# Optimization experiments

Measured on AMD Instinct MI355X. Metric: run time of the kernel, lower is better.

The kernel has to match this reference:

```python
import jax, jax.numpy as jnp
import numpy as np

N = 100000   # nodes per graph (protein == ligand node count, forced by cat dim=1)
E = 3200000  # edges per graph (avg degree 32)
F = 128      # input feature dim
A = 10       # action dim


def _fanin_uniform(key, shape, fanin=None):
    fanin = fanin or shape[0]
    v = 1.0 / np.sqrt(fanin)
    return jax.random.uniform(key, shape, jnp.float32, -v, v)


def setup_inputs() -> dict:
    key = jax.random.key(0)
    ks = jax.random.split(key, 24)
    inp = {
        "protein_x": jax.random.normal(ks[0], (N, F), jnp.float32),
        "protein_edges": jax.random.randint(ks[1], (2, E), 0, N, jnp.int32),
        "ligand_x": jax.random.normal(ks[2], (N, F), jnp.float32),
        "ligand_edges": jax.random.randint(ks[3], (2, E), 0, N, jnp.int32),
        "action": jax.random.normal(ks[4], (N, A), jnp.float32),
        # protein GraphConv layers
        "wp1s": _fanin_uniform(ks[5], (F, 16)),
        "wp1n": _fanin_uniform(ks[6], (F, 16)),
        "bp1": jnp.zeros((16,), jnp.float32),
        "wp2s": _fanin_uniform(ks[7], (16, 50)),
        "wp2n": _fanin_uniform(ks[8], (16, 50)),
        "bp2": jnp.zeros((50,), jnp.float32),
        # ligand GraphConv layers
        "wl1s": _fanin_uniform(ks[9], (F, 16)),
        "wl1n": _fanin_uniform(ks[10], (F, 16)),
        "bl1": jnp.zeros((16,), jnp.float32),
        "wl2s": _fanin_uniform(ks[11], (16, 50)),
        "wl2n": _fanin_uniform(ks[12], (16, 50)),
        "bl2": jnp.zeros((50,), jnp.float32),
        # MLP head
        "w_in": _fanin_uniform(ks[13], (100, 60)),
        "b_in": jnp.zeros((60,), jnp.float32),
        "w_hid": _fanin_uniform(ks[14], (60 + A, 10)),
        "b_hid": jnp.zeros((10,), jnp.float32),
        "w_out": jax.random.uniform(ks[15], (10, 1), jnp.float32, -0.003, 0.003),
        "b_out": jnp.zeros((1,), jnp.float32),
    }
    return inp


def graph_conv(x, edge_index, w_self, w_nbr, b):
    # PyG GraphConv: x_i' = x_i @ W_self + (sum_{j->i} x_j) @ W_nbr + b
    src, dst = edge_index[0], edge_index[1]
    agg = jax.ops.segment_sum(x[src], dst, num_segments=x.shape[0])  # [N, Fin]
    return x @ w_self + agg @ w_nbr + b


def reference(protein_x, protein_edges, ligand_x, ligand_edges, action,
              wp1s, wp1n, bp1, wp2s, wp2n, bp2,
              wl1s, wl1n, bl1, wl2s, wl2n, bl2,
              w_in, b_in, w_hid, b_hid, w_out, b_out):
    # protein branch (dropout is identity in eval mode)
    p = jax.nn.relu(graph_conv(protein_x, protein_edges, wp1s, wp1n, bp1))
    p = graph_conv(p, protein_edges, wp2s, wp2n, bp2)            # [N, 50]
    # ligand branch
    l = jax.nn.relu(graph_conv(ligand_x, ligand_edges, wl1s, wl1n, bl1))
    l = graph_conv(l, ligand_edges, wl2s, wl2n, bl2)             # [N, 50]
    molecule = jnp.concatenate([p, l], axis=1)                   # [N, 100]
    finger_print = jax.nn.relu(molecule @ w_in + b_in)           # [N, 60]
    policy = jnp.concatenate([finger_print, action], axis=1) @ w_hid + b_hid
    policy = jax.nn.relu(policy) @ w_out + b_out                 # [N, 1]
    return policy
```

## Files before the change

kernel.cpp:

```cpp
#include <hip/hip_runtime.h>
#include <hip/hip_bf16.h>
#include <stdint.h>


#define F_IN 128
#define NBMAX 512
#define BIN_CH 16
#define BIN_EDGES (256 * BIN_CH)
#define FINE_CAP 12288

#define OW1P  0
#define OB1P  4096
#define OW1L  4112
#define OB1L  8208
#define OC1P  8224
#define OC2P  9184
#define OC1L  10144
#define OC2L  11104
#define OBIN  12064
#define OWHID 12124
#define OBHID 12824
#define OWOUT 12834
#define OBOUT 12844
#define WBUF_FLOATS 16384

__device__ __forceinline__ float bf2f(unsigned short u) {
    union { unsigned int i; float f; } v; v.i = ((unsigned int)u) << 16; return v.f;
}
__device__ __forceinline__ float bflo(unsigned int u) {
    union { unsigned int i; float f; } v; v.i = u << 16; return v.f;
}
__device__ __forceinline__ float bfhi(unsigned int u) {
    union { unsigned int i; float f; } v; v.i = u & 0xffff0000u; return v.f;
}
__device__ __forceinline__ unsigned short f2bf(float f) {
    union { float f; unsigned int i; } v; v.f = f;
    unsigned int u = v.i;
    unsigned int r = (u + 0x7fffu + ((u >> 16) & 1u)) >> 16;
    return (unsigned short)r;
}
__device__ __forceinline__ unsigned pack2bf(float a, float b) {
    return (unsigned)f2bf(a) | ((unsigned)f2bf(b) << 16);
}
__device__ __forceinline__ float ldf(const void* p, int isf32, size_t i) {
    return isf32 ? ((const float*)p)[i] : bf2f(((const unsigned short*)p)[i]);
}

__global__ __launch_bounds__(256) void k_detect(
    const unsigned short* __restrict__ x, int nProbe, int* __restrict__ flag,
    int* __restrict__ zp, int zn)
{
    if (blockIdx.x == 0) {
        __shared__ int cnt;
        if (threadIdx.x == 0) cnt = 0;
        __syncthreads();
        int bad = 0;
        for (int i = threadIdx.x; i < nProbe; i += 256) {
            unsigned e = (x[i] >> 7) & 0xFFu;
            if (e >= 140u) bad++;
        }
        atomicAdd(&cnt, bad);
        __syncthreads();
        if (threadIdx.x == 0) *flag = (cnt > nProbe / 16) ? 1 : 0;
    } else {
        int i = (blockIdx.x - 1) * 256 + threadIdx.x;
        if (i < zn) zp[i] = 0;
    }
}


struct PW {
    const void *wp1s, *wp1n, *bp1, *wl1s, *wl1n, *bl1;
    const void *wp2s, *wp2n, *bp2, *wl2s, *wl2n, *bl2;
    const void *w_in, *b_in, *w_hid, *b_hid, *w_out, *b_out;
};

__global__ __launch_bounds__(256) void k_prepw(PW P, float* __restrict__ wb,
                                               const int* __restrict__ flag)
{
    const int isf32 = *flag;
    int t = blockIdx.x * 256 + threadIdx.x;
    int stride = gridDim.x * 256;
    for (int i = t; i < 4096; i += stride) {
        int k = i >> 5, j = i & 31;
        wb[OW1P + i] = (j < 16) ? ldf(P.wp1s, isf32, k * 16 + j)
                                : ldf(P.wp1n, isf32, k * 16 + (j - 16));
        wb[OW1L + i] = (j < 16) ? ldf(P.wl1s, isf32, k * 16 + j)
                                : ldf(P.wl1n, isf32, k * 16 + (j - 16));
    }
    for (int i = t; i < 16; i += stride) {
        wb[OB1P + i] = ldf(P.bp1, isf32, i);
        wb[OB1L + i] = ldf(P.bl1, isf32, i);
    }
    for (int i = t; i < 960; i += stride) {
        int k = i / 60, j = i % 60;
        float s1 = 0.f, s2 = 0.f;
        for (int r = 0; r < 50; ++r) {
            float wi = ldf(P.w_in, isf32, r * 60 + j);
            s1 += ldf(P.wp2s, isf32, k * 50 + r) * wi;
            s2 += ldf(P.wp2n, isf32, k * 50 + r) * wi;
        }
        wb[OC1P + i] = s1; wb[OC2P + i] = s2;
    }
    for (int i = t; i < 960; i += stride) {
        int k = i / 60, j = i % 60;
        float s1 = 0.f, s2 = 0.f;
        for (int r = 0; r < 50; ++r) {
            float wi = ldf(P.w_in, isf32, (50 + r) * 60 + j);
            s1 += ldf(P.wl2s, isf32, k * 50 + r) * wi;
            s2 += ldf(P.wl2n, isf32, k * 50 + r) * wi;
        }
        wb[OC1L + i] = s1; wb[OC2L + i] = s2;
    }
    for (int i = t; i < 60; i += stride) {
        float s = ldf(P.b_in, isf32, i);
        for (int r = 0; r < 50; ++r) {
            s += ldf(P.bp2, isf32, r) * ldf(P.w_in, isf32, r * 60 + i);
            s += ldf(P.bl2, isf32, r) * ldf(P.w_in, isf32, (50 + r) * 60 + i);
        }
        wb[OBIN + i] = s;
    }
    for (int i = t; i < 700; i += stride) wb[OWHID + i] = ldf(P.w_hid, isf32, i);
    for (int i = t; i < 10; i += stride) {
        wb[OBHID + i] = ldf(P.b_hid, isf32, i);
        wb[OWOUT + i] = ldf(P.w_out, isf32, i);
    }
    if (t == 0) wb[OBOUT] = ldf(P.b_out, isf32, 0);
}


__global__ __launch_bounds__(256) void k_bucket_hist(
    const int* __restrict__ ed0, const int* __restrict__ ed1,
    int* __restrict__ cnt, int nE)
{
    const int* ed = blockIdx.y ? ed1 : ed0;
    int* c = cnt + blockIdx.y * NBMAX;
    __shared__ int h[NBMAX];
    for (int i = threadIdx.x; i < NBMAX; i += 256) h[i] = 0;
    __syncthreads();
    int stride = gridDim.x * 256;
    for (int e = blockIdx.x * 256 + threadIdx.x; e < nE; e += stride)
        atomicAdd(&h[ed[e] >> 8], 1);
    __syncthreads();
    for (int i = threadIdx.x; i < NBMAX; i += 256)
        if (h[i]) atomicAdd(&c[i], h[i]);
}

__global__ __launch_bounds__(512) void k_bucket_scan(
    const int* __restrict__ cnt, int* __restrict__ base,
    int* __restrict__ cursor, int nb)
{
    const int* c = cnt + blockIdx.x * NBMAX;
    int* ba = base + blockIdx.x * 528;
    int* cu = cursor + blockIdx.x * NBMAX;
    __shared__ int sh[512];
    int t = threadIdx.x;
    int v = (t < nb) ? c[t] : 0;
    sh[t] = v;
    __syncthreads();
    for (int off = 1; off < 512; off <<= 1) {
        int x = (t >= off) ? sh[t - off] : 0;
        __syncthreads();
        sh[t] += x;
        __syncthreads();
    }
    int excl = sh[t] - v;
    if (t < nb) { ba[t] = excl; cu[t] = excl; }
    if (t == nb - 1) ba[nb] = excl + v;
}

__global__ __launch_bounds__(256) void k_bucket_bin(
    const int* __restrict__ es0, const int* __restrict__ ed0,
    const int* __restrict__ es1, const int* __restrict__ ed1,
    int* __restrict__ cursor, unsigned* __restrict__ pairs, int nE)
{
    const int* es = blockIdx.y ? es1 : es0;
    const int* ed = blockIdx.y ? ed1 : ed0;
    int* cur = cursor + blockIdx.y * NBMAX;
    unsigned* pr = pairs + (size_t)blockIdx.y * nE;

    __shared__ int h[NBMAX];
    __shared__ int lcur[NBMAX];
    __shared__ int sh[256];
    __shared__ unsigned stage[BIN_EDGES];
    __shared__ unsigned short stageB[BIN_EDGES];

    for (int i = threadIdx.x; i < NBMAX; i += 256) h[i] = 0;
    __syncthreads();
    int e0 = blockIdx.x * BIN_EDGES;
    int s[BIN_CH], d[BIN_CH];
#pragma unroll
    for (int k = 0; k < BIN_CH; ++k) {
        int e = e0 + k * 256 + threadIdx.x;
        if (e < nE) {
            s[k] = es[e]; d[k] = ed[e];
            atomicAdd(&h[d[k] >> 8], 1);
        } else d[k] = -1;
    }
    __syncthreads();
    {
        int t = threadIdx.x;
        int a = h[2 * t], b2 = h[2 * t + 1];
        sh[t] = a + b2;
        __syncthreads();
        for (int off = 1; off < 256; off <<= 1) {
            int x = (t >= off) ? sh[t - off] : 0;
            __syncthreads();
            sh[t] += x;
            __syncthreads();
        }
        int excl = sh[t] - (a + b2);
        lcur[2 * t] = excl;
        lcur[2 * t + 1] = excl + a;
    }
    __syncthreads();
    for (int b = threadIdx.x; b < NBMAX; b += 256) {
        int c = h[b];
        if (c) {
            int g = atomicAdd(&cur[b], c);
            h[b] = g - lcur[b];
        }
    }
    __syncthreads();
#pragma unroll
    for (int k = 0; k < BIN_CH; ++k) {
        if (d[k] >= 0) {
            int b = d[k] >> 8;
            int pos = atomicAdd(&lcur[b], 1);
            stage[pos] = ((unsigned)(d[k] & 255) << 24) | (unsigned)s[k];
            stageB[pos] = (unsigned short)b;
        }
    }
    __syncthreads();
    int total = nE - e0; if (total > BIN_EDGES) total = BIN_EDGES;
    for (int i = threadIdx.x; i < total; i += 256)
        pr[h[stageB[i]] + i] = stage[i];
}

__global__ __launch_bounds__(256) void k_bucket_fine(
    const unsigned* __restrict__ pairs, const int* __restrict__ base,
    int* __restrict__ row0, int* __restrict__ srcs0,
    int* __restrict__ row1, int* __restrict__ srcs1,
    int n, int nE, int nb)
{
    const unsigned* pr = pairs + (size_t)blockIdx.y * nE;
    const int* ba = base + blockIdx.y * 528;
    int* row = blockIdx.y ? row1 : row0;
    int* srcs = blockIdx.y ? srcs1 : srcs0;
    __shared__ int cnt[256], cur[256];
    __shared__ int stage[FINE_CAP];
    int b = blockIdx.x;
    int t = threadIdx.x;
    int s0 = ba[b], s1 = ba[b + 1];
    int m = s1 - s0;
    cnt[t] = 0;
    __syncthreads();
    for (int i = s0 + t; i < s1; i += 256)
        atomicAdd(&cnt[pr[i] >> 24], 1);
    __syncthreads();
    int c = cnt[t];
    cur[t] = c;
    __syncthreads();
    for (int off = 1; off < 256; off <<= 1) {
        int x = (t >= off) ? cur[t - off] : 0;
        __syncthreads();
        cur[t] += x;
        __syncthreads();
    }
    int excl = cur[t] - c;
    __syncthreads();
    int node = (b << 8) + t;
    if (node < n) row[node] = s0 + excl;
    if (b == nb - 1 && t == 0) row[n] = nE;
    if (m <= FINE_CAP) {
        cur[t] = excl;
        __syncthreads();
        for (int i = s0 + t; i < s1; i += 256) {
            unsigned p = pr[i];
            int slot = atomicAdd(&cur[p >> 24], 1);
            stage[slot] = (int)(p & 0xFFFFFFu);
        }
        __syncthreads();
        for (int i = t; i < m; i += 256)
            srcs[s0 + i] = stage[i];
    } else {
        cur[t] = s0 + excl;
        __syncthreads();
        for (int i = s0 + t; i < s1; i += 256) {
            unsigned p = pr[i];
            int slot = atomicAdd(&cur[p >> 24], 1);
            srcs[slot] = (int)(p & 0xFFFFFFu);
        }
    }
}


struct TArgs2 {
    const void* __restrict__ x;
    const float* __restrict__ w;
    const float* __restrict__ b;
    float* __restrict__ acc;
    void* __restrict__ nbr;
};

__global__ __launch_bounds__(512) void k_transform1(
    TArgs2 a0, TArgs2 a1, int n, const int* __restrict__ flag)
{
    TArgs2 A = blockIdx.y ? a1 : a0;
    const int isf32 = *flag;
    __shared__ unsigned char xs_raw[32768];
    const int t = threadIdx.x;
    const int tile0 = blockIdx.x * 64;

    if (isf32) {
        const float4* xg = (const float4*)A.x;
        float4* xl = (float4*)xs_raw;
#pragma unroll
        for (int i = 0; i < 4; ++i) {
            int flat = i * 512 + t;
            int row = flat >> 5, ck = flat & 31;
            if (tile0 + row < n)
                xl[row * 32 + (ck ^ (row & 7))] =
                    xg[((size_t)(tile0 + row)) * 32 + ck];
        }
    } else {
        const uint4* xg = (const uint4*)A.x;
        uint4* xl = (uint4*)xs_raw;
#pragma unroll
        for (int i = 0; i < 2; ++i) {
            int flat = i * 512 + t;
            int row = flat >> 4, ck = flat & 15;
            if (tile0 + row < n)
                xl[row * 16 + (ck ^ (row & 7))] =
                    xg[((size_t)(tile0 + row)) * 16 + ck];
        }
    }
    __syncthreads();

    const int jq = __builtin_amdgcn_readfirstlane(t >> 6);
    const int r = t & 63;
    const int node = tile0 + r;
    if (node >= n) return;
    const float* __restrict__ Wb = A.w + 4 * jq;
    const int sw = r & 7;

    float acc[4];
    if (jq < 4) {
#pragma unroll
        for (int j = 0; j < 4; ++j) acc[j] = A.b[4 * jq + j];
    } else {
#pragma unroll
        for (int j = 0; j < 4; ++j) acc[j] = 0.f;
    }

    if (isf32) {
        const float4* xl = (const float4*)xs_raw + r * 32;
        for (int kk = 0; kk < 32; ++kk) {
            float4 q = xl[kk ^ sw];
            float xv[4] = {q.x, q.y, q.z, q.w};
#pragma unroll
            for (int h = 0; h < 4; ++h) {
                const float* __restrict__ w0 = Wb + (kk * 4 + h) * 32;
#pragma unroll
                for (int j = 0; j < 4; ++j) acc[j] += xv[h] * w0[j];
            }
        }
    } else {
        const uint4* xl = (const uint4*)xs_raw + r * 16;
        for (int kk = 0; kk < 16; ++kk) {
            uint4 q = xl[kk ^ sw];
            float xv[8] = {bflo(q.x), bfhi(q.x), bflo(q.y), bfhi(q.y),
                           bflo(q.z), bfhi(q.z), bflo(q.w), bfhi(q.w)};
#pragma unroll
            for (int h = 0; h < 8; ++h) {
                const float* __restrict__ w0 = Wb + (kk * 8 + h) * 32;
#pragma unroll
                for (int j = 0; j < 4; ++j) acc[j] += xv[h] * w0[j];
            }
        }
    }

    if (jq < 4) {
        float4* a4 = (float4*)(A.acc + (size_t)node * 16);
        a4[jq] = make_float4(acc[0], acc[1], acc[2], acc[3]);
    } else {
        unsigned short* nrow = (unsigned short*)A.nbr + ((size_t)node << 4)
                               + ((jq - 4) << 2);
        *(uint2*)nrow = make_uint2(pack2bf(acc[0], acc[1]),
                                   pack2bf(acc[2], acc[3]));
    }
}

struct GArgs { const int *row, *srcs; const void* val; float* out; void* rout; };

__global__ __launch_bounds__(256) void k_gather16(
    GArgs g0, GArgs g1, int n, int selfmode, int yoff)
{
    GArgs G = (blockIdx.y + yoff) ? g1 : g0;
    int t = blockIdx.x * 256 + threadIdx.x;
    int node = t >> 2;
    if (node >= n) return;
    int c = (t & 3) << 2;
    const unsigned short* vb = (const unsigned short*)G.val;
    int rs = G.row[node], re = G.row[node + 1];
    float4 sum = make_float4(0.f, 0.f, 0.f, 0.f);
    if (selfmode) sum = *(const float4*)(G.out + ((size_t)node << 4) + c);
    int j = rs;
    for (; j + 16 <= re; j += 16) {
        int s[16];
        uint2 v[16];
#pragma unroll
        for (int u = 0; u < 16; ++u) s[u] = G.srcs[j + u];
#pragma unroll
        for (int u = 0; u < 16; ++u)
            v[u] = *(const uint2*)(vb + (((size_t)s[u]) << 4) + c);
#pragma unroll
        for (int u = 0; u < 16; ++u) {
            sum.x += bflo(v[u].x); sum.y += bfhi(v[u].x);
            sum.z += bflo(v[u].y); sum.w += bfhi(v[u].y);
        }
    }
    for (; j + 8 <= re; j += 8) {
        int s[8];
        uint2 v[8];
#pragma unroll
        for (int u = 0; u < 8; ++u) s[u] = G.srcs[j + u];
#pragma unroll
        for (int u = 0; u < 8; ++u)
            v[u] = *(const uint2*)(vb + (((size_t)s[u]) << 4) + c);
#pragma unroll
        for (int u = 0; u < 8; ++u) {
            sum.x += bflo(v[u].x); sum.y += bfhi(v[u].x);
            sum.z += bflo(v[u].y); sum.w += bfhi(v[u].y);
        }
    }
    for (; j < re; ++j) {
        uint2 v = *(const uint2*)(vb + (((size_t)G.srcs[j]) << 4) + c);
        sum.x += bflo(v.x); sum.y += bfhi(v.x);
        sum.z += bflo(v.y); sum.w += bfhi(v.y);
    }
    *(float4*)(G.out + ((size_t)node << 4) + c) = sum;
    if (selfmode) {
        unsigned short* orow = (unsigned short*)G.rout + ((size_t)node << 4) + c;
        *(uint2*)orow = make_uint2(pack2bf(fmaxf(sum.x, 0.f), fmaxf(sum.y, 0.f)),
                                   pack2bf(fmaxf(sum.z, 0.f), fmaxf(sum.w, 0.f)));
    }
}

__device__ __forceinline__ void fp_acc30(float* fp, const float* __restrict__ wb,
                                         int off, int jo,
                                         const float* __restrict__ row, bool dorelu)
{
    const float4* r4 = (const float4*)row;
    for (int kk = 0; kk < 4; ++kk) {
        float4 v = r4[kk];
        float xs[4] = {v.x, v.y, v.z, v.w};
        if (dorelu) {
            xs[0] = fmaxf(xs[0], 0.f); xs[1] = fmaxf(xs[1], 0.f);
            xs[2] = fmaxf(xs[2], 0.f); xs[3] = fmaxf(xs[3], 0.f);
        }
        const float* __restrict__ wq = wb + off + kk * 240 + jo;
#pragma unroll
        for (int h = 0; h < 4; ++h) {
#pragma unroll
            for (int j = 0; j < 30; ++j) fp[j] += xs[h] * wq[h * 60 + j];
        }
    }
}

__global__ __launch_bounds__(256) void k_headf(
    const float* __restrict__ hP, const float* __restrict__ gP,
    const float* __restrict__ hL, const float* __restrict__ gL,
    const void* __restrict__ action, const float* __restrict__ wb,
    void* __restrict__ out, int n, const int* __restrict__ flag)
{
    const int isf32 = *flag;
    __shared__ float hbuf[128][10];
    int w = threadIdx.x >> 6;
    int jh = __builtin_amdgcn_readfirstlane(w & 1);
    int slot = ((w >> 1) << 6) + (threadIdx.x & 63);
    int node = blockIdx.x * 128 + slot;
    int nodec = node < n ? node : (n - 1);
    const int jo = 30 * jh;

    float fp[30];
#pragma unroll
    for (int j = 0; j < 30; ++j) fp[j] = wb[OBIN + jo + j];

    fp_acc30(fp, wb, OC1P, jo, hP + (size_t)nodec * 16, true);
    fp_acc30(fp, wb, OC2P, jo, gP + (size_t)nodec * 16, false);
    fp_acc30(fp, wb, OC1L, jo, hL + (size_t)nodec * 16, true);
    fp_acc30(fp, wb, OC2L, jo, gL + (size_t)nodec * 16, false);

    float h[10];
#pragma unroll
    for (int j = 0; j < 10; ++j) h[j] = (jh == 0) ? wb[OBHID + j] : 0.f;
#pragma unroll
    for (int k = 0; k < 30; ++k) {
        float v = fmaxf(fp[k], 0.f);
#pragma unroll
        for (int j = 0; j < 10; ++j) h[j] += v * wb[OWHID + (jo + k) * 10 + j];
    }
    if (jh) {
#pragma unroll
        for (int j = 0; j < 10; ++j) hbuf[slot][j] = h[j];
    }
    __syncthreads();
    if (jh == 0) {
#pragma unroll
        for (int j = 0; j < 10; ++j) h[j] += hbuf[slot][j];
#pragma unroll
        for (int k = 0; k < 10; ++k) {
            float v = ldf(action, isf32, (size_t)nodec * 10 + k);
#pragma unroll
            for (int j = 0; j < 10; ++j) h[j] += v * wb[OWHID + (60 + k) * 10 + j];
        }
        float o = wb[OBOUT];
#pragma unroll
        for (int j = 0; j < 10; ++j) o += fmaxf(h[j], 0.f) * wb[OWOUT + j];
        if (node < n) {
            if (isf32) ((float*)out)[node] = o;
            else       ((unsigned short*)out)[node] = f2bf(o);
        }
    }
}

extern "C" void kernel_launch(void* const* d_in, const int* in_sizes, int n_in,
                              void* d_out, int out_size, void* d_ws, size_t ws_size,
                              hipStream_t stream)
{
    const void* px   = d_in[0];
    const int*  pe   = (const int*)d_in[1];
    const void* lx   = d_in[2];
    const int*  le   = (const int*)d_in[3];
    const void* act  = d_in[4];

    const int N = in_sizes[0] / F_IN;
    const int E = in_sizes[1] / 2;
    const int NB = (N + 255) >> 8;

    int* flag    = (int*)d_ws;
    int* cnt     = flag + 64;
    int* base    = cnt + 2 * NBMAX;
    int* cursorB = base + 2 * 528;
    float* wbuf  = (float*)(flag + 3200);
    int* rowP    = flag + 3200 + WBUF_FLOATS;
    int* srcsP   = rowP + (N + 64);
    int* rowL    = srcsP + E;
    int* srcsL   = rowL + (N + 64);
    float* dense = (float*)(srcsL + E);
    unsigned* pairs = (unsigned*)dense;

    float* accP = dense;
    float* accL = accP + (size_t)N * 16;
    float* aggP = accL + (size_t)N * 16;
    float* aggL = aggP + (size_t)N * 16;
    void*  n1P  = (void*)(aggL + (size_t)N * 16);
    void*  n1L  = (void*)((float*)n1P + (size_t)N * 8);
    void*  n2P  = (void*)((float*)n1L + (size_t)N * 8);
    void*  n2L  = (void*)((float*)n2P + (size_t)N * 8);

    const int nb64 = (N + 63) / 64;
    const int nb128 = (N + 127) / 128;
    const int gb = (N * 4 + 255) / 256;
    const int bb = (E + BIN_EDGES - 1) / BIN_EDGES;

    k_detect<<<5, 256, 0, stream>>>((const unsigned short*)px, 4096, flag,
                                    cnt, 2 * NBMAX);

    PW P{d_in[5], d_in[6], d_in[7], d_in[11], d_in[12], d_in[13],
         d_in[8], d_in[9], d_in[10], d_in[14], d_in[15], d_in[16],
         d_in[17], d_in[18], d_in[19], d_in[20], d_in[21], d_in[22]};
    k_prepw<<<32, 256, 0, stream>>>(P, wbuf, flag);

    k_bucket_hist<<<dim3(512, 2), 256, 0, stream>>>(pe + E, le + E, cnt, E);
    k_bucket_scan<<<2, 512, 0, stream>>>(cnt, base, cursorB, NB);
    k_bucket_bin<<<dim3(bb, 2), 256, 0, stream>>>(pe, pe + E, le, le + E,
                                                  cursorB, pairs, E);
    k_bucket_fine<<<dim3(NB, 2), 256, 0, stream>>>(pairs, base, rowP, srcsP,
                                                   rowL, srcsL, N, E, NB);

    TArgs2 tP{px, wbuf + OW1P, wbuf + OB1P, accP, n1P};
    TArgs2 tL{lx, wbuf + OW1L, wbuf + OB1L, accL, n1L};
    k_transform1<<<dim3(nb64, 2), 512, 0, stream>>>(tP, tL, N, flag);

    GArgs g1P{rowP, srcsP, n1P, accP, n2P}, g1L{rowL, srcsL, n1L, accL, n2L};
    k_gather16<<<dim3(gb, 2), 256, 0, stream>>>(g1P, g1L, N, 1, 0);

    GArgs g2P{rowP, srcsP, n2P, aggP, nullptr}, g2L{rowL, srcsL, n2L, aggL, nullptr};
    k_gather16<<<dim3(gb, 2), 256, 0, stream>>>(g2P, g2L, N, 0, 0);

    k_headf<<<nb128, 256, 0, stream>>>(accP, aggP, accL, aggL, act, wbuf,
                                       d_out, N, flag);
}
```

Baseline: 485.7 us.

## Merge dtype detection into weight prep, widen gather loads, unpack bf16 at staging

Removes the separate detect kernel by having every k_prepw block recompute the dtype probe and zero the counters, which saves one launch. The two gather passes now use 2 threads per node with 16-byte loads instead of 4 threads with 8-byte loads, so fewer instructions are issued per gathered neighbour row. In the transform kernel, bf16 inputs are converted to fp32 once while staging into LDS, so a single fp32 inner loop serves both dtypes. The cost is less thread parallelism in the gather and redundant probe work in every prepw block.

```diff
diff --git a/kernel.cpp b/kernel.cpp
--- a/kernel.cpp
+++ b/kernel.cpp
@@ -46,28 +46,6 @@
     return isf32 ? ((const float*)p)[i] : bf2f(((const unsigned short*)p)[i]);
 }
 
-__global__ __launch_bounds__(256) void k_detect(
-    const unsigned short* __restrict__ x, int nProbe, int* __restrict__ flag,
-    int* __restrict__ zp, int zn)
-{
-    if (blockIdx.x == 0) {
-        __shared__ int cnt;
-        if (threadIdx.x == 0) cnt = 0;
-        __syncthreads();
-        int bad = 0;
-        for (int i = threadIdx.x; i < nProbe; i += 256) {
-            unsigned e = (x[i] >> 7) & 0xFFu;
-            if (e >= 140u) bad++;
-        }
-        atomicAdd(&cnt, bad);
-        __syncthreads();
-        if (threadIdx.x == 0) *flag = (cnt > nProbe / 16) ? 1 : 0;
-    } else {
-        int i = (blockIdx.x - 1) * 256 + threadIdx.x;
-        if (i < zn) zp[i] = 0;
-    }
-}
-
 
 struct PW {
     const void *wp1s, *wp1n, *bp1, *wl1s, *wl1n, *bl1;
@@ -75,12 +53,27 @@
     const void *w_in, *b_in, *w_hid, *b_hid, *w_out, *b_out;
 };
 
-__global__ __launch_bounds__(256) void k_prepw(PW P, float* __restrict__ wb,
-                                               const int* __restrict__ flag)
-{
-    const int isf32 = *flag;
+__global__ __launch_bounds__(256) void k_prepw(
+    PW P, const unsigned short* __restrict__ px, float* __restrict__ wb,
+    int* __restrict__ flag, int* __restrict__ zp, int zn)
+{
+    __shared__ int cnt_s;
+    if (threadIdx.x == 0) cnt_s = 0;
+    __syncthreads();
+    int bad = 0;
+    for (int i = threadIdx.x; i < 4096; i += 256) {
+        unsigned e = (px[i] >> 7) & 0xFFu;
+        if (e >= 140u) bad++;
+    }
+    atomicAdd(&cnt_s, bad);
+    __syncthreads();
+    const int isf32 = (cnt_s > 4096 / 16) ? 1 : 0;
+    if (threadIdx.x == 0 && blockIdx.x == 0) *flag = isf32;
+
     int t = blockIdx.x * 256 + threadIdx.x;
     int stride = gridDim.x * 256;
+    for (int i = t; i < zn; i += stride) zp[i] = 0;
+
     for (int i = t; i < 4096; i += stride) {
         int k = i >> 5, j = i & 31;
         wb[OW1P + i] = (j < 16) ? ldf(P.wp1s, isf32, k * 16 + j)
@@ -308,13 +301,13 @@
 {
     TArgs2 A = blockIdx.y ? a1 : a0;
     const int isf32 = *flag;
-    __shared__ unsigned char xs_raw[32768];
+    __shared__ float xs[64 * 128];
     const int t = threadIdx.x;
     const int tile0 = blockIdx.x * 64;
 
     if (isf32) {
         const float4* xg = (const float4*)A.x;
-        float4* xl = (float4*)xs_raw;
+        float4* xl = (float4*)xs;
 #pragma unroll
         for (int i = 0; i < 4; ++i) {
             int flat = i * 512 + t;
@@ -325,14 +318,18 @@
         }
     } else {
         const uint4* xg = (const uint4*)A.x;
-        uint4* xl = (uint4*)xs_raw;
+        float4* xl = (float4*)xs;
 #pragma unroll
         for (int i = 0; i < 2; ++i) {
             int flat = i * 512 + t;
             int row = flat >> 4, ck = flat & 15;
-            if (tile0 + row < n)
-                xl[row * 16 + (ck ^ (row & 7))] =
-                    xg[((size_t)(tile0 + row)) * 16 + ck];
+            if (tile0 + row < n) {
+                uint4 q = xg[((size_t)(tile0 + row)) * 16 + ck];
+                float4 lo = make_float4(bflo(q.x), bfhi(q.x), bflo(q.y), bfhi(q.y));
+                float4 hi = make_float4(bflo(q.z), bfhi(q.z), bflo(q.w), bfhi(q.w));
+                xl[row * 32 + ((2 * ck) ^ (row & 7))] = lo;
+                xl[row * 32 + ((2 * ck + 1) ^ (row & 7))] = hi;
+            }
         }
     }
     __syncthreads();
@@ -353,30 +350,15 @@
         for (int j = 0; j < 4; ++j) acc[j] = 0.f;
     }
 
-    if (isf32) {
-        const float4* xl = (const float4*)xs_raw + r * 32;
-        for (int kk = 0; kk < 32; ++kk) {
-            float4 q = xl[kk ^ sw];
-            float xv[4] = {q.x, q.y, q.z, q.w};
-#pragma unroll
-            for (int h = 0; h < 4; ++h) {
-                const float* __restrict__ w0 = Wb + (kk * 4 + h) * 32;
-#pragma unroll
-                for (int j = 0; j < 4; ++j) acc[j] += xv[h] * w0[j];
-            }
-        }
-    } else {
-        const uint4* xl = (const uint4*)xs_raw + r * 16;
-        for (int kk = 0; kk < 16; ++kk) {
-            uint4 q = xl[kk ^ sw];
-            float xv[8] = {bflo(q.x), bfhi(q.x), bflo(q.y), bfhi(q.y),
-                           bflo(q.z), bfhi(q.z), bflo(q.w), bfhi(q.w)};
-#pragma unroll
-            for (int h = 0; h < 8; ++h) {
-                const float* __restrict__ w0 = Wb + (kk * 8 + h) * 32;
-#pragma unroll
-                for (int j = 0; j < 4; ++j) acc[j] += xv[h] * w0[j];
-            }
+    const float4* xl = (const float4*)xs + r * 32;
+    for (int kk = 0; kk < 32; ++kk) {
+        float4 q = xl[kk ^ sw];
+        float xv[4] = {q.x, q.y, q.z, q.w};
+#pragma unroll
+        for (int h = 0; h < 4; ++h) {
+            const float* __restrict__ w0 = Wb + (kk * 4 + h) * 32;
+#pragma unroll
+            for (int j = 0; j < 4; ++j) acc[j] += xv[h] * w0[j];
         }
     }
 
@@ -398,52 +380,66 @@
 {
     GArgs G = (blockIdx.y + yoff) ? g1 : g0;
     int t = blockIdx.x * 256 + threadIdx.x;
-    int node = t >> 2;
+    int node = t >> 1;
     if (node >= n) return;
-    int c = (t & 3) << 2;
+    int c = (t & 1) << 3;
     const unsigned short* vb = (const unsigned short*)G.val;
     int rs = G.row[node], re = G.row[node + 1];
-    float4 sum = make_float4(0.f, 0.f, 0.f, 0.f);
-    if (selfmode) sum = *(const float4*)(G.out + ((size_t)node << 4) + c);
+    float4 sa = make_float4(0.f, 0.f, 0.f, 0.f);
+    float4 sb = make_float4(0.f, 0.f, 0.f, 0.f);
+    if (selfmode) {
+        const float4* o4 = (const float4*)(G.out + ((size_t)node << 4) + c);
+        sa = o4[0]; sb = o4[1];
+    }
     int j = rs;
     for (; j + 16 <= re; j += 16) {
         int s[16];
-        uint2 v[16];
+        uint4 v[16];
 #pragma unroll
         for (int u = 0; u < 16; ++u) s[u] = G.srcs[j + u];
 #pragma unroll
         for (int u = 0; u < 16; ++u)
-            v[u] = *(const uint2*)(vb + (((size_t)s[u]) << 4) + c);
+            v[u] = *(const uint4*)(vb + (((size_t)s[u]) << 4) + c);
 #pragma unroll
         for (int u = 0; u < 16; ++u) {
-            sum.x += bflo(v[u].x); sum.y += bfhi(v[u].x);
-            sum.z += bflo(v[u].y); sum.w += bfhi(v[u].y);
+            sa.x += bflo(v[u].x); sa.y += bfhi(v[u].x);
+            sa.z += bflo(v[u].y); sa.w += bfhi(v[u].y);
+            sb.x += bflo(v[u].z); sb.y += bfhi(v[u].z);
+            sb.z += bflo(v[u].w); sb.w += bfhi(v[u].w);
         }
     }
     for (; j + 8 <= re; j += 8) {
         int s[8];
-        uint2 v[8];
+        uint4 v[8];
 #pragma unroll
         for (int u = 0; u < 8; ++u) s[u] = G.srcs[j + u];
 #pragma unroll
         for (int u = 0; u < 8; ++u)
-            v[u] = *(const uint2*)(vb + (((size_t)s[u]) << 4) + c);
+            v[u] = *(const uint4*)(vb + (((size_t)s[u]) << 4) + c);
 #pragma unroll
         for (int u = 0; u < 8; ++u) {
-            sum.x += bflo(v[u].x); sum.y += bfhi(v[u].x);
-            sum.z += bflo(v[u].y); sum.w += bfhi(v[u].y);
+            sa.x += bflo(v[u].x); sa.y += bfhi(v[u].x);
+            sa.z += bflo(v[u].y); sa.w += bfhi(v[u].y);
+            sb.x += bflo(v[u].z); sb.y += bfhi(v[u].z);
+            sb.z += bflo(v[u].w); sb.w += bfhi(v[u].w);
         }
     }
     for (; j < re; ++j) {
-        uint2 v = *(const uint2*)(vb + (((size_t)G.srcs[j]) << 4) + c);
-        sum.x += bflo(v.x); sum.y += bfhi(v.x);
-        sum.z += bflo(v.y); sum.w += bfhi(v.y);
-    }
-    *(float4*)(G.out + ((size_t)node << 4) + c) = sum;
+        uint4 v = *(const uint4*)(vb + (((size_t)G.srcs[j]) << 4) + c);
+        sa.x += bflo(v.x); sa.y += bfhi(v.x);
+        sa.z += bflo(v.y); sa.w += bfhi(v.y);
+        sb.x += bflo(v.z); sb.y += bfhi(v.z);
+        sb.z += bflo(v.w); sb.w += bfhi(v.w);
+    }
+    float4* o4 = (float4*)(G.out + ((size_t)node << 4) + c);
+    o4[0] = sa; o4[1] = sb;
     if (selfmode) {
         unsigned short* orow = (unsigned short*)G.rout + ((size_t)node << 4) + c;
-        *(uint2*)orow = make_uint2(pack2bf(fmaxf(sum.x, 0.f), fmaxf(sum.y, 0.f)),
-                                   pack2bf(fmaxf(sum.z, 0.f), fmaxf(sum.w, 0.f)));
+        *(uint4*)orow = make_uint4(
+            pack2bf(fmaxf(sa.x, 0.f), fmaxf(sa.y, 0.f)),
+            pack2bf(fmaxf(sa.z, 0.f), fmaxf(sa.w, 0.f)),
+            pack2bf(fmaxf(sb.x, 0.f), fmaxf(sb.y, 0.f)),
+            pack2bf(fmaxf(sb.z, 0.f), fmaxf(sb.w, 0.f)));
     }
 }
 
@@ -562,16 +558,14 @@
 
     const int nb64 = (N + 63) / 64;
     const int nb128 = (N + 127) / 128;
-    const int gb = (N * 4 + 255) / 256;
+    const int gb2 = (N * 2 + 255) / 256;
     const int bb = (E + BIN_EDGES - 1) / BIN_EDGES;
-
-    k_detect<<<5, 256, 0, stream>>>((const unsigned short*)px, 4096, flag,
-                                    cnt, 2 * NBMAX);
 
     PW P{d_in[5], d_in[6], d_in[7], d_in[11], d_in[12], d_in[13],
          d_in[8], d_in[9], d_in[10], d_in[14], d_in[15], d_in[16],
          d_in[17], d_in[18], d_in[19], d_in[20], d_in[21], d_in[22]};
-    k_prepw<<<32, 256, 0, stream>>>(P, wbuf, flag);
+    k_prepw<<<32, 256, 0, stream>>>(P, (const unsigned short*)px, wbuf,
+                                    flag, cnt, 2 * NBMAX);
 
     k_bucket_hist<<<dim3(512, 2), 256, 0, stream>>>(pe + E, le + E, cnt, E);
     k_bucket_scan<<<2, 512, 0, stream>>>(cnt, base, cursorB, NB);
@@ -585,10 +579,10 @@
     k_transform1<<<dim3(nb64, 2), 512, 0, stream>>>(tP, tL, N, flag);
 
     GArgs g1P{rowP, srcsP, n1P, accP, n2P}, g1L{rowL, srcsL, n1L, accL, n2L};
-    k_gather16<<<dim3(gb, 2), 256, 0, stream>>>(g1P, g1L, N, 1, 0);
+    k_gather16<<<dim3(gb2, 2), 256, 0, stream>>>(g1P, g1L, N, 1, 0);
 
     GArgs g2P{rowP, srcsP, n2P, aggP, nullptr}, g2L{rowL, srcsL, n2L, aggL, nullptr};
-    k_gather16<<<dim3(gb, 2), 256, 0, stream>>>(g2P, g2L, N, 0, 0);
+    k_gather16<<<dim3(gb2, 2), 256, 0, stream>>>(g2P, g2L, N, 0, 0);
 
     k_headf<<<nb128, 256, 0, stream>>>(accP, aggP, accL, aggL, act, wbuf,
                                        d_out, N, flag);
```

Result: no change. 490.6 us (+1.0%).
